# Kernel tuning notes

Measured on AMD Instinct MI355X. Metric: run time of the kernel, lower is better.

Reference implementation:

```python
import jax, jax.numpy as jnp
import numpy as np

NUM_HEADS = 8
NUM_GROUPS = 8
EPS = 1e-5


def group_norm(x, scale, bias):
    # x: [B, C, H, W]; GroupNorm with NUM_GROUPS groups, per-channel affine.
    B, C, H, W = x.shape
    xg = x.reshape(B, NUM_GROUPS, C // NUM_GROUPS, H, W)
    mean = jnp.mean(xg, axis=(2, 3, 4), keepdims=True)
    var = jnp.var(xg, axis=(2, 3, 4), keepdims=True)
    xg = (xg - mean) * jax.lax.rsqrt(var + EPS)
    xn = xg.reshape(B, C, H, W)
    return xn * scale[None, :, None, None] + bias[None, :, None, None]


def setup_inputs() -> dict:
    key = jax.random.key(0)
    ks = jax.random.split(key, 4)
    B, C, H, W = 8, 256, 32, 32
    x = jax.random.normal(ks[0], (B, C, H, W), dtype=jnp.float32)
    gn_scale = jnp.ones((C,), dtype=jnp.float32)
    gn_bias = jnp.zeros((C,), dtype=jnp.float32)
    w_qkv = jax.random.normal(ks[1], (3 * C, C), dtype=jnp.float32) * (1.0 / np.sqrt(C))
    b_qkv = jnp.zeros((3 * C,), dtype=jnp.float32)
    w_out = jax.random.normal(ks[2], (C, C), dtype=jnp.float32) * (1.0 / np.sqrt(C))
    b_out = jnp.zeros((C,), dtype=jnp.float32)
    return {"x": x, "gn_scale": gn_scale, "gn_bias": gn_bias,
            "w_qkv": w_qkv, "b_qkv": b_qkv, "w_out": w_out, "b_out": b_out}


def reference(x, gn_scale, gn_bias, w_qkv, b_qkv, w_out, b_out):
    B, C, H, W = x.shape
    hd = C // NUM_HEADS  # head_dim
    N = H * W

    h = group_norm(x, gn_scale, gn_bias)
    # 1x1 conv == channel matmul: [B, 3C, H, W]
    qkv = jnp.einsum('oc,bchw->bohw', w_qkv, h) + b_qkv[None, :, None, None]
    q, k, v = jnp.split(qkv, 3, axis=1)
    # [B, heads, head_dim, N]
    q = q.reshape(B, NUM_HEADS, hd, N)
    k = k.reshape(B, NUM_HEADS, hd, N)
    v = v.reshape(B, NUM_HEADS, hd, N)

    scale = 1.0 / np.sqrt(hd).astype(np.float32)
    attn = jnp.einsum('bhdn,bhdm->bhnm', q, k) * scale  # [B, h, N, N]
    attn = jax.nn.softmax(attn, axis=-1)
    out = jnp.einsum('bhnm,bhdm->bhdn', attn, v)  # [B, h, hd, N]
    out = out.reshape(B, C, H, W)
    out = jnp.einsum('oc,bchw->bohw', w_out, out) + b_out[None, :, None, None]
    return x + out
```

## Files before the change

kernel.cpp:

```cpp
#include <hip/hip_runtime.h>
#include <hip/hip_bf16.h>
#include <math.h>

#define BB 8
#define CC 256
#define NN 1024
#define HEADS 8
#define HDIM 32
#define NGRP 8

using bf16x8 = __attribute__((ext_vector_type(8))) short;
using f32x4  = __attribute__((ext_vector_type(4))) float;

#if __has_builtin(__builtin_amdgcn_exp2f)
#define EXP2(x) __builtin_amdgcn_exp2f(x)
#else
#define EXP2(x) exp2f(x)
#endif

#define SCL_Q_LOG2E 0.2550348892803828f

static __device__ __forceinline__ ushort f2bf(float x) {
  union { __hip_bfloat16 b; ushort u; } c;
  c.b = __float2bfloat16(x);
  return c.u;
}

__global__ __launch_bounds__(256) void wcast_kernel(
    const float* __restrict__ wqkv, const float* __restrict__ wout,
    ushort* __restrict__ wbf)
{
  const int gid = blockIdx.x * 256 + threadIdx.x;
  const int e8 = gid * 8;
  const float* src = (e8 < 196608) ? (wqkv + e8) : (wout + (e8 - 196608));
  const float4 a = *(const float4*)src;
  const float4 c = *(const float4*)(src + 4);
  union { uint4 v; ushort s[8]; } o;
  o.s[0] = f2bf(a.x); o.s[1] = f2bf(a.y); o.s[2] = f2bf(a.z); o.s[3] = f2bf(a.w);
  o.s[4] = f2bf(c.x); o.s[5] = f2bf(c.y); o.s[6] = f2bf(c.z); o.s[7] = f2bf(c.w);
  *(uint4*)(wbf + e8) = o.v;
}

__global__ __launch_bounds__(256) void gn_stats1(
    const float* __restrict__ x, float2* __restrict__ part)
{
  const int p = blockIdx.x, t = threadIdx.x;
  const float4* src = (const float4*)x + (size_t)p * 512;
  const float4 a = src[t], b = src[t + 256];
  float s  = a.x + a.y + a.z + a.w + b.x + b.y + b.z + b.w;
  float ss = a.x*a.x + a.y*a.y + a.z*a.z + a.w*a.w
           + b.x*b.x + b.y*b.y + b.z*b.z + b.w*b.w;
#pragma unroll
  for (int off = 32; off > 0; off >>= 1) {
    s  += __shfl_down(s, off);
    ss += __shfl_down(ss, off);
  }
  __shared__ float rs[4], rss[4];
  const int wid = t >> 6, lane = t & 63;
  if (lane == 0) { rs[wid] = s; rss[wid] = ss; }
  __syncthreads();
  if (t == 0) {
    float2 o;
    o.x = rs[0] + rs[1] + rs[2] + rs[3];
    o.y = rss[0] + rss[1] + rss[2] + rss[3];
    part[p] = o;
  }
}

__global__ __launch_bounds__(64) void gn_stats2(
    const float2* __restrict__ part, float2* __restrict__ stats)
{
  const int g = blockIdx.x, l = threadIdx.x;
  float s = 0.f, ss = 0.f;
  if (l < 16) { const float2 pp = part[g * 16 + l]; s = pp.x; ss = pp.y; }
#pragma unroll
  for (int off = 8; off > 0; off >>= 1) {
    s  += __shfl_down(s, off);
    ss += __shfl_down(ss, off);
  }
  if (l == 0) {
    const float mean = s * (1.f / 32768.f);
    const float var = ss * (1.f / 32768.f) - mean * mean;
    float2 o; o.x = mean; o.y = rsqrtf(var + 1e-5f);
    stats[g] = o;
  }
}

__global__ __launch_bounds__(256) void gnt_kernel(
    const float* __restrict__ x, const float2* __restrict__ stats,
    const float* __restrict__ gns, const float* __restrict__ gnb,
    ushort* __restrict__ hT)
{
  __shared__ ushort Ls[64 * 68];
  const int t = threadIdx.x;
  const int b = blockIdx.z;
  const int c0 = blockIdx.y << 6, n0 = blockIdx.x << 6;

#pragma unroll
  for (int li = 0; li < 4; ++li) {
    const int id = t + (li << 8);
    const int row = id >> 4, col4 = id & 15;
    const int c = c0 + row;
    const float2 st = stats[b * 8 + (c >> 5)];
    const float sc = gns[c] * st.y;
    const float sh = gnb[c] - st.x * sc;
    const float4 v = *(const float4*)(x + ((size_t)b * CC + c) * NN + n0 + col4 * 4);
    const int nb = col4 * 4;
    Ls[(nb + 0) * 68 + row] = f2bf(v.x * sc + sh);
    Ls[(nb + 1) * 68 + row] = f2bf(v.y * sc + sh);
    Ls[(nb + 2) * 68 + row] = f2bf(v.z * sc + sh);
    Ls[(nb + 3) * 68 + row] = f2bf(v.w * sc + sh);
  }
  __syncthreads();
#pragma unroll
  for (int li = 0; li < 2; ++li) {
    const int id = t + (li << 8);
    const int nR = id >> 3, cP = id & 7;
    union { uint4 v; ushort4 s[2]; } ov;
    ov.s[0] = *(const ushort4*)&Ls[nR * 68 + cP * 8];
    ov.s[1] = *(const ushort4*)&Ls[nR * 68 + cP * 8 + 4];
    *(uint4*)(hT + ((size_t)b * NN + n0 + nR) * CC + c0 + cP * 8) = ov.v;
  }
}

template <int MODE>
__global__ __launch_bounds__(256) void conv_mfma_kernel(
    const ushort* __restrict__ Wbf, const float* __restrict__ bias,
    const ushort* __restrict__ X, const float* __restrict__ xres,
    ushort* __restrict__ qT, ushort* __restrict__ kT, ushort* __restrict__ vN,
    float* __restrict__ out)
{
  const int t = threadIdx.x;
  const int w = t >> 6, l = t & 63;
  const int lg = l >> 4, lr = l & 15;
  const int wr = w >> 1, wc = w & 1;
  const int b = blockIdx.z;
  const int o0 = blockIdx.y << 6, n0 = blockIdx.x << 6;

  __shared__ ushort Ws[64][72];
  __shared__ ushort Xs[64][72];

  union FragU { ushort4 u[2]; bf16x8 f; };
  f32x4 acc[2][2] = {};

  const ushort* Xb = X + (size_t)b * 1024 * 256;

  for (int k0 = 0; k0 < 256; k0 += 64) {
    __syncthreads();
#pragma unroll
    for (int li = 0; li < 2; ++li) {
      const int id = t + (li << 8);
      const int rr = id >> 3, c8 = id & 7;
      const uint4 wv = *(const uint4*)(Wbf + (size_t)(o0 + rr) * 256 + k0 + c8 * 8);
      *(uint4*)&Ws[rr][c8 * 8] = wv;
      const uint4 xv = *(const uint4*)(Xb + (size_t)(n0 + rr) * 256 + k0 + c8 * 8);
      *(uint4*)&Xs[rr][c8 * 8] = xv;
    }
    __syncthreads();

    FragU af[2][2], xf[2][2];
#pragma unroll
    for (int i = 0; i < 2; ++i)
#pragma unroll
      for (int kc = 0; kc < 2; ++kc) {
        const ushort* p = &Ws[wr * 32 + i * 16 + lr][kc * 32 + lg * 4];
        af[i][kc].u[0] = *(const ushort4*)p;
        af[i][kc].u[1] = *(const ushort4*)(p + 16);
        const ushort* q = &Xs[wc * 32 + i * 16 + lr][kc * 32 + lg * 4];
        xf[i][kc].u[0] = *(const ushort4*)q;
        xf[i][kc].u[1] = *(const ushort4*)(q + 16);
      }
#pragma unroll
    for (int ms = 0; ms < 2; ++ms)
#pragma unroll
      for (int ns = 0; ns < 2; ++ns) {
        acc[ms][ns] = __builtin_amdgcn_mfma_f32_16x16x32_bf16(af[ms][0].f, xf[ns][0].f, acc[ms][ns], 0, 0, 0);
        acc[ms][ns] = __builtin_amdgcn_mfma_f32_16x16x32_bf16(af[ms][1].f, xf[ns][1].f, acc[ms][ns], 0, 0, 0);
      }
  }

  if (MODE == 0) {
    const int sec = o0 >> 8;
    const float scl = (sec == 0) ? SCL_Q_LOG2E : 1.0f;
#pragma unroll
    for (int ms = 0; ms < 2; ++ms) {
      const int ob = o0 + wr * 32 + ms * 16 + lg * 4;
      const float4 b4 = *(const float4*)(bias + ob);
      const int oo = ob & 255;
      const int hh = oo >> 5, d0 = oo & 31;
      const int bh = b * 8 + hh;
#pragma unroll
      for (int ns = 0; ns < 2; ++ns) {
        const int n = n0 + wc * 32 + ns * 16 + lr;
        float v0 = (acc[ms][ns][0] + b4.x) * scl;
        float v1 = (acc[ms][ns][1] + b4.y) * scl;
        float v2 = (acc[ms][ns][2] + b4.z) * scl;
        float v3 = (acc[ms][ns][3] + b4.w) * scl;
        if (sec < 2) {
          ushort* dst = (sec == 0) ? qT : kT;
          ushort4 w4 = {f2bf(v0), f2bf(v1), f2bf(v2), f2bf(v3)};
          *(ushort4*)&dst[((size_t)bh * 1024 + n) * 32 + d0] = w4;
        } else {
          vN[((size_t)bh * 32 + d0 + 0) * 1024 + n] = f2bf(v0);
          vN[((size_t)bh * 32 + d0 + 1) * 1024 + n] = f2bf(v1);
          vN[((size_t)bh * 32 + d0 + 2) * 1024 + n] = f2bf(v2);
          vN[((size_t)bh * 32 + d0 + 3) * 1024 + n] = f2bf(v3);
        }
      }
    }
  } else {
#pragma unroll
    for (int ms = 0; ms < 2; ++ms) {
      const int ob = o0 + wr * 32 + ms * 16 + lg * 4;
      const float4 b4 = *(const float4*)(bias + ob);
#pragma unroll
      for (int ns = 0; ns < 2; ++ns) {
        const int n = n0 + wc * 32 + ns * 16 + lr;
        const size_t i0 = ((size_t)b * 256 + ob) * 1024 + n;
        out[i0]          = acc[ms][ns][0] + b4.x + xres[i0];
        out[i0 + 1024]   = acc[ms][ns][1] + b4.y + xres[i0 + 1024];
        out[i0 + 2048]   = acc[ms][ns][2] + b4.z + xres[i0 + 2048];
        out[i0 + 3072]   = acc[ms][ns][3] + b4.w + xres[i0 + 3072];
      }
    }
  }
}

__global__ __launch_bounds__(256) void attn_kernel(
    const ushort* __restrict__ qT, const ushort* __restrict__ kT,
    const ushort* __restrict__ vN, ushort* __restrict__ aoT)
{
  const int t = threadIdx.x;
  const int w = t >> 6, l = t & 63;
  const int lg = l >> 4, lr = l & 15;
  const int bh = blockIdx.y;
  const int b = bh >> 3, hh = bh & 7;
  const int qbase = blockIdx.x << 6;

  __shared__ ushort Ks[128][40];
  __shared__ ushort Vs[32][136];

  union FragU { ushort4 u[2]; bf16x8 f; };

  FragU qf;
  {
    const ushort* Qp = qT + (((size_t)bh * 1024 + qbase + w * 16 + lr) * 32) + lg * 4;
    qf.u[0] = *(const ushort4*)Qp;
    qf.u[1] = *(const ushort4*)(Qp + 16);
  }

  f32x4 accO[2] = {};
  float m_st = -1e30f, l_st = 0.f;

  const ushort* Kbh = kT + (size_t)bh * 1024 * 32;
  const ushort* Vbh = vN + (size_t)bh * 32 * 1024;
  const uint4* Kt = (const uint4*)Kbh;
  const int vd = t >> 4, vm8 = (t & 15) * 8;

  uint4 kr0, kr1, vr0, vr1;
  {
    kr0 = Kt[t];
    kr1 = Kt[t + 256];
    vr0 = *(const uint4*)(Vbh + (size_t)vd * 1024 + vm8);
    vr1 = *(const uint4*)(Vbh + (size_t)(vd + 16) * 1024 + vm8);
  }

  for (int m0 = 0; m0 < NN; m0 += 128) {
    __syncthreads();
    *(uint4*)&Ks[t >> 2][(t & 3) * 8] = kr0;
    *(uint4*)&Ks[64 + (t >> 2)][(t & 3) * 8] = kr1;
    *(uint4*)&Vs[vd][vm8] = vr0;
    *(uint4*)&Vs[vd + 16][vm8] = vr1;
    __syncthreads();

    if (m0 + 128 < NN) {
      const int mn = m0 + 128;
      kr0 = Kt[mn * 4 + t];
      kr1 = Kt[mn * 4 + t + 256];
      vr0 = *(const uint4*)(Vbh + (size_t)vd * 1024 + mn + vm8);
      vr1 = *(const uint4*)(Vbh + (size_t)(vd + 16) * 1024 + mn + vm8);
    }

    f32x4 s[8];
#pragma unroll
    for (int ms = 0; ms < 8; ++ms) {
      FragU kf;
      const ushort* kp = &Ks[ms * 16 + lr][lg * 4];
      kf.u[0] = *(const ushort4*)kp;
      kf.u[1] = *(const ushort4*)(kp + 16);
      f32x4 z = {0.f, 0.f, 0.f, 0.f};
      s[ms] = __builtin_amdgcn_mfma_f32_16x16x32_bf16(kf.f, qf.f, z, 0, 0, 0);
    }

    float mx = s[0][0];
#pragma unroll
    for (int ms = 0; ms < 8; ++ms)
#pragma unroll
      for (int r = 0; r < 4; ++r) mx = fmaxf(mx, s[ms][r]);
    mx = fmaxf(mx, __shfl_xor(mx, 16));
    mx = fmaxf(mx, __shfl_xor(mx, 32));
    const float mnew = fmaxf(m_st, mx);
    const float c = EXP2(m_st - mnew);
    m_st = mnew;
    float ls = 0.f;
#pragma unroll
    for (int ms = 0; ms < 8; ++ms)
#pragma unroll
      for (int r = 0; r < 4; ++r) {
        const float p = EXP2(s[ms][r] - mnew);
        s[ms][r] = p;
        ls += p;
      }
    ls += __shfl_xor(ls, 16);
    ls += __shfl_xor(ls, 32);
    l_st = l_st * c + ls;
#pragma unroll
    for (int dt = 0; dt < 2; ++dt)
#pragma unroll
      for (int r = 0; r < 4; ++r) accO[dt][r] *= c;

    bf16x8 pb[4];
#pragma unroll
    for (int mc = 0; mc < 4; ++mc) {
      bf16x8 f;
#pragma unroll
      for (int r = 0; r < 4; ++r) {
        f[r]     = (short)f2bf(s[2 * mc][r]);
        f[r + 4] = (short)f2bf(s[2 * mc + 1][r]);
      }
      pb[mc] = f;
    }

#pragma unroll
    for (int dt = 0; dt < 2; ++dt) {
#pragma unroll
      for (int mc = 0; mc < 4; ++mc) {
        FragU vf;
        const ushort* vp = &Vs[dt * 16 + lr][mc * 32 + lg * 4];
        vf.u[0] = *(const ushort4*)vp;
        vf.u[1] = *(const ushort4*)(vp + 16);
        accO[dt] = __builtin_amdgcn_mfma_f32_16x16x32_bf16(vf.f, pb[mc], accO[dt], 0, 0, 0);
      }
    }
  }

  const float inv = 1.f / l_st;
  const int n = qbase + w * 16 + lr;
  ushort* ap = aoT + ((size_t)b * 1024 + n) * 256 + hh * 32 + lg * 4;
#pragma unroll
  for (int dt = 0; dt < 2; ++dt) {
    ushort4 w4;
    w4.x = f2bf(accO[dt][0] * inv);
    w4.y = f2bf(accO[dt][1] * inv);
    w4.z = f2bf(accO[dt][2] * inv);
    w4.w = f2bf(accO[dt][3] * inv);
    *(ushort4*)(ap + dt * 16) = w4;
  }
}

extern "C" void kernel_launch(void* const* d_in, const int* in_sizes, int n_in,
                              void* d_out, int out_size, void* d_ws, size_t ws_size,
                              hipStream_t stream)
{
  const float* x    = (const float*)d_in[0];
  const float* gns  = (const float*)d_in[1];
  const float* gnb  = (const float*)d_in[2];
  const float* wqkv = (const float*)d_in[3];
  const float* bqkv = (const float*)d_in[4];
  const float* wout = (const float*)d_in[5];
  const float* bout = (const float*)d_in[6];
  float* out = (float*)d_out;

  char* ws = (char*)d_ws;
  ushort* hT    = (ushort*)(ws);
  ushort* qT    = (ushort*)(ws + (4u << 20));
  ushort* kT    = (ushort*)(ws + (8u << 20));
  ushort* vN    = (ushort*)(ws + (12u << 20));
  ushort* aoT   = (ushort*)(ws + (16u << 20));
  ushort* wbf   = (ushort*)(ws + (20u << 20));
  float2* part  = (float2*)(ws + (21u << 20));
  float2* stats = (float2*)(ws + (21u << 20) + 8192);

  wcast_kernel<<<dim3(128), dim3(256), 0, stream>>>(wqkv, wout, wbf);
  gn_stats1<<<dim3(1024), dim3(256), 0, stream>>>(x, part);
  gn_stats2<<<dim3(64), dim3(64), 0, stream>>>(part, stats);
  gnt_kernel<<<dim3(16, 4, 8), dim3(256), 0, stream>>>(x, stats, gns, gnb, hT);
  conv_mfma_kernel<0><<<dim3(16, 12, 8), dim3(256), 0, stream>>>(
      wbf, bqkv, hT, nullptr, qT, kT, vN, nullptr);
  attn_kernel<<<dim3(16, 64), dim3(256), 0, stream>>>(qT, kT, vN, aoT);
  conv_mfma_kernel<1><<<dim3(16, 4, 8), dim3(256), 0, stream>>>(
      wbf + 768 * 256, bout, aoT, x, nullptr, nullptr, nullptr, out);
}
```

Measured before the change: 128.1 us.

## Fuse weight cast and GN stats into consumers, stage stores through LDS

Removes the separate weight-cast and group-norm finalize kernels. The bf16 weight conversion moves into the conv tile loader, and the stats reduction moves into gnt_kernel, cutting two launches. The QKV conv epilogue now goes through shared memory so q/k/v writes are wide and coalesced, with q/k stored in a split half-head layout the attention kernel reads directly. The attention output is also staged through LDS for 16-byte stores, and the softmax max/sum reductions are split into independent chains for more ILP. The cost is that each conv block redoes the fp32-to-bf16 weight conversion and reads fp32 weights, which doubles weight traffic.

```diff
diff --git a/kernel.cpp b/kernel.cpp
--- a/kernel.cpp
+++ b/kernel.cpp
@@ -24,21 +24,6 @@
   union { __hip_bfloat16 b; ushort u; } c;
   c.b = __float2bfloat16(x);
   return c.u;
-}
-
-__global__ __launch_bounds__(256) void wcast_kernel(
-    const float* __restrict__ wqkv, const float* __restrict__ wout,
-    ushort* __restrict__ wbf)
-{
-  const int gid = blockIdx.x * 256 + threadIdx.x;
-  const int e8 = gid * 8;
-  const float* src = (e8 < 196608) ? (wqkv + e8) : (wout + (e8 - 196608));
-  const float4 a = *(const float4*)src;
-  const float4 c = *(const float4*)(src + 4);
-  union { uint4 v; ushort s[8]; } o;
-  o.s[0] = f2bf(a.x); o.s[1] = f2bf(a.y); o.s[2] = f2bf(a.z); o.s[3] = f2bf(a.w);
-  o.s[4] = f2bf(c.x); o.s[5] = f2bf(c.y); o.s[6] = f2bf(c.z); o.s[7] = f2bf(c.w);
-  *(uint4*)(wbf + e8) = o.v;
 }
 
 __global__ __launch_bounds__(256) void gn_stats1(
@@ -67,41 +52,41 @@
   }
 }
 
-__global__ __launch_bounds__(64) void gn_stats2(
-    const float2* __restrict__ part, float2* __restrict__ stats)
-{
-  const int g = blockIdx.x, l = threadIdx.x;
-  float s = 0.f, ss = 0.f;
-  if (l < 16) { const float2 pp = part[g * 16 + l]; s = pp.x; ss = pp.y; }
-#pragma unroll
-  for (int off = 8; off > 0; off >>= 1) {
-    s  += __shfl_down(s, off);
-    ss += __shfl_down(ss, off);
-  }
-  if (l == 0) {
-    const float mean = s * (1.f / 32768.f);
-    const float var = ss * (1.f / 32768.f) - mean * mean;
-    float2 o; o.x = mean; o.y = rsqrtf(var + 1e-5f);
-    stats[g] = o;
-  }
-}
-
 __global__ __launch_bounds__(256) void gnt_kernel(
-    const float* __restrict__ x, const float2* __restrict__ stats,
+    const float* __restrict__ x, const float2* __restrict__ part,
     const float* __restrict__ gns, const float* __restrict__ gnb,
     ushort* __restrict__ hT)
 {
   __shared__ ushort Ls[64 * 68];
+  __shared__ float2 gstat[2];
   const int t = threadIdx.x;
   const int b = blockIdx.z;
   const int c0 = blockIdx.y << 6, n0 = blockIdx.x << 6;
+
+  if (t < 32) {
+    const int gsel = t >> 4, ci = t & 15;
+    const float2 pp = part[((b * 8) + (blockIdx.y << 1) + gsel) * 16 + ci];
+    float s = pp.x, ss = pp.y;
+#pragma unroll
+    for (int off = 8; off > 0; off >>= 1) {
+      s  += __shfl_down(s, off, 16);
+      ss += __shfl_down(ss, off, 16);
+    }
+    if (ci == 0) {
+      const float mean = s * (1.f / 32768.f);
+      const float var = ss * (1.f / 32768.f) - mean * mean;
+      float2 o; o.x = mean; o.y = rsqrtf(var + 1e-5f);
+      gstat[gsel] = o;
+    }
+  }
+  __syncthreads();
 
 #pragma unroll
   for (int li = 0; li < 4; ++li) {
     const int id = t + (li << 8);
     const int row = id >> 4, col4 = id & 15;
     const int c = c0 + row;
-    const float2 st = stats[b * 8 + (c >> 5)];
+    const float2 st = gstat[row >> 5];
     const float sc = gns[c] * st.y;
     const float sh = gnb[c] - st.x * sc;
     const float4 v = *(const float4*)(x + ((size_t)b * CC + c) * NN + n0 + col4 * 4);
@@ -125,9 +110,9 @@
 
 template <int MODE>
 __global__ __launch_bounds__(256) void conv_mfma_kernel(
-    const ushort* __restrict__ Wbf, const float* __restrict__ bias,
+    const float* __restrict__ W32, const float* __restrict__ bias,
     const ushort* __restrict__ X, const float* __restrict__ xres,
-    ushort* __restrict__ qT, ushort* __restrict__ kT, ushort* __restrict__ vN,
+    ushort* __restrict__ qT2, ushort* __restrict__ kT2, ushort* __restrict__ vN,
     float* __restrict__ out)
 {
   const int t = threadIdx.x;
@@ -151,8 +136,13 @@
     for (int li = 0; li < 2; ++li) {
       const int id = t + (li << 8);
       const int rr = id >> 3, c8 = id & 7;
-      const uint4 wv = *(const uint4*)(Wbf + (size_t)(o0 + rr) * 256 + k0 + c8 * 8);
-      *(uint4*)&Ws[rr][c8 * 8] = wv;
+      const float* wsrc = W32 + (size_t)(o0 + rr) * 256 + k0 + c8 * 8;
+      const float4 wa = *(const float4*)wsrc;
+      const float4 wb = *(const float4*)(wsrc + 4);
+      union { uint4 v; ushort s[8]; } wv;
+      wv.s[0] = f2bf(wa.x); wv.s[1] = f2bf(wa.y); wv.s[2] = f2bf(wa.z); wv.s[3] = f2bf(wa.w);
+      wv.s[4] = f2bf(wb.x); wv.s[5] = f2bf(wb.y); wv.s[6] = f2bf(wb.z); wv.s[7] = f2bf(wb.w);
+      *(uint4*)&Ws[rr][c8 * 8] = wv.v;
       const uint4 xv = *(const uint4*)(Xb + (size_t)(n0 + rr) * 256 + k0 + c8 * 8);
       *(uint4*)&Xs[rr][c8 * 8] = xv;
     }
@@ -181,32 +171,47 @@
 
   if (MODE == 0) {
     const int sec = o0 >> 8;
+    const int oin = o0 & 255;
     const float scl = (sec == 0) ? SCL_Q_LOG2E : 1.0f;
+    ushort* Lp = &Xs[0][0];
+    __syncthreads();
 #pragma unroll
     for (int ms = 0; ms < 2; ++ms) {
       const int ob = o0 + wr * 32 + ms * 16 + lg * 4;
       const float4 b4 = *(const float4*)(bias + ob);
-      const int oo = ob & 255;
-      const int hh = oo >> 5, d0 = oo & 31;
-      const int bh = b * 8 + hh;
+      const int ol = wr * 32 + ms * 16 + lg * 4;
 #pragma unroll
       for (int ns = 0; ns < 2; ++ns) {
-        const int n = n0 + wc * 32 + ns * 16 + lr;
-        float v0 = (acc[ms][ns][0] + b4.x) * scl;
-        float v1 = (acc[ms][ns][1] + b4.y) * scl;
-        float v2 = (acc[ms][ns][2] + b4.z) * scl;
-        float v3 = (acc[ms][ns][3] + b4.w) * scl;
-        if (sec < 2) {
-          ushort* dst = (sec == 0) ? qT : kT;
-          ushort4 w4 = {f2bf(v0), f2bf(v1), f2bf(v2), f2bf(v3)};
-          *(ushort4*)&dst[((size_t)bh * 1024 + n) * 32 + d0] = w4;
-        } else {
-          vN[((size_t)bh * 32 + d0 + 0) * 1024 + n] = f2bf(v0);
-          vN[((size_t)bh * 32 + d0 + 1) * 1024 + n] = f2bf(v1);
-          vN[((size_t)bh * 32 + d0 + 2) * 1024 + n] = f2bf(v2);
-          vN[((size_t)bh * 32 + d0 + 3) * 1024 + n] = f2bf(v3);
-        }
-      }
+        const int nl = wc * 32 + ns * 16 + lr;
+        Lp[(ol + 0) * 68 + nl] = f2bf((acc[ms][ns][0] + b4.x) * scl);
+        Lp[(ol + 1) * 68 + nl] = f2bf((acc[ms][ns][1] + b4.y) * scl);
+        Lp[(ol + 2) * 68 + nl] = f2bf((acc[ms][ns][2] + b4.z) * scl);
+        Lp[(ol + 3) * 68 + nl] = f2bf((acc[ms][ns][3] + b4.w) * scl);
+      }
+    }
+    __syncthreads();
+    if (sec < 2) {
+      ushort* dst = (sec == 0) ? qT2 : kT2;
+      const int nl = t & 63, hd = t >> 6;
+      const int hl = hd >> 1, dh = hd & 1;
+      const int bh = b * 8 + (oin >> 5) + hl;
+      union { uint4 v[2]; ushort s[16]; } o;
+#pragma unroll
+      for (int j = 0; j < 16; ++j)
+        o.s[j] = Lp[(hl * 32 + dh * 16 + j) * 68 + nl];
+      uint4* dp = (uint4*)(dst + (((size_t)bh * 2 + dh) * 1024 + n0 + nl) * 16);
+      dp[0] = o.v[0];
+      dp[1] = o.v[1];
+    } else {
+      const int r = t >> 2, p = t & 3;
+      const int oo = oin + r, hh = oo >> 5, d0 = oo & 31;
+      union { uint4 v[2]; ushort4 s[4]; } o;
+#pragma unroll
+      for (int j = 0; j < 4; ++j)
+        o.s[j] = *(const ushort4*)&Lp[r * 68 + p * 16 + j * 4];
+      uint4* dp = (uint4*)(vN + (((size_t)b * 8 + hh) * 32 + d0) * 1024 + n0 + p * 16);
+      dp[0] = o.v[0];
+      dp[1] = o.v[1];
     }
   } else {
 #pragma unroll
@@ -227,7 +232,7 @@
 }
 
 __global__ __launch_bounds__(256) void attn_kernel(
-    const ushort* __restrict__ qT, const ushort* __restrict__ kT,
+    const ushort* __restrict__ qT2, const ushort* __restrict__ kT2,
     const ushort* __restrict__ vN, ushort* __restrict__ aoT)
 {
   const int t = threadIdx.x;
@@ -242,41 +247,42 @@
 
   union FragU { ushort4 u[2]; bf16x8 f; };
 
+  const ushort* Qb2 = qT2 + (size_t)bh * 2 * 1024 * 16;
+  const ushort* Kb2 = kT2 + (size_t)bh * 2 * 1024 * 16;
+  const ushort* Vbh = vN + (size_t)bh * 32 * 1024;
+
   FragU qf;
   {
-    const ushort* Qp = qT + (((size_t)bh * 1024 + qbase + w * 16 + lr) * 32) + lg * 4;
-    qf.u[0] = *(const ushort4*)Qp;
-    qf.u[1] = *(const ushort4*)(Qp + 16);
+    const int qn = qbase + w * 16 + lr;
+    qf.u[0] = *(const ushort4*)(Qb2 + (size_t)qn * 16 + lg * 4);
+    qf.u[1] = *(const ushort4*)(Qb2 + (size_t)(1024 + qn) * 16 + lg * 4);
   }
 
   f32x4 accO[2] = {};
   float m_st = -1e30f, l_st = 0.f;
 
-  const ushort* Kbh = kT + (size_t)bh * 1024 * 32;
-  const ushort* Vbh = vN + (size_t)bh * 32 * 1024;
-  const uint4* Kt = (const uint4*)Kbh;
+  const int km = t >> 2, kq = t & 3;
+  const size_t koff0 = ((size_t)(kq >> 1) * 1024 + km) * 16 + (kq & 1) * 8;
   const int vd = t >> 4, vm8 = (t & 15) * 8;
 
   uint4 kr0, kr1, vr0, vr1;
-  {
-    kr0 = Kt[t];
-    kr1 = Kt[t + 256];
-    vr0 = *(const uint4*)(Vbh + (size_t)vd * 1024 + vm8);
-    vr1 = *(const uint4*)(Vbh + (size_t)(vd + 16) * 1024 + vm8);
-  }
+  kr0 = *(const uint4*)(Kb2 + koff0);
+  kr1 = *(const uint4*)(Kb2 + koff0 + 64 * 16);
+  vr0 = *(const uint4*)(Vbh + (size_t)vd * 1024 + vm8);
+  vr1 = *(const uint4*)(Vbh + (size_t)(vd + 16) * 1024 + vm8);
 
   for (int m0 = 0; m0 < NN; m0 += 128) {
     __syncthreads();
-    *(uint4*)&Ks[t >> 2][(t & 3) * 8] = kr0;
-    *(uint4*)&Ks[64 + (t >> 2)][(t & 3) * 8] = kr1;
+    *(uint4*)&Ks[km][kq * 8] = kr0;
+    *(uint4*)&Ks[64 + km][kq * 8] = kr1;
     *(uint4*)&Vs[vd][vm8] = vr0;
     *(uint4*)&Vs[vd + 16][vm8] = vr1;
     __syncthreads();
 
     if (m0 + 128 < NN) {
       const int mn = m0 + 128;
-      kr0 = Kt[mn * 4 + t];
-      kr1 = Kt[mn * 4 + t + 256];
+      kr0 = *(const uint4*)(Kb2 + koff0 + (size_t)mn * 16);
+      kr1 = *(const uint4*)(Kb2 + koff0 + (size_t)(mn + 64) * 16);
       vr0 = *(const uint4*)(Vbh + (size_t)vd * 1024 + mn + vm8);
       vr1 = *(const uint4*)(Vbh + (size_t)(vd + 16) * 1024 + mn + vm8);
     }
@@ -292,25 +298,32 @@
       s[ms] = __builtin_amdgcn_mfma_f32_16x16x32_bf16(kf.f, qf.f, z, 0, 0, 0);
     }
 
-    float mx = s[0][0];
-#pragma unroll
-    for (int ms = 0; ms < 8; ++ms)
-#pragma unroll
-      for (int r = 0; r < 4; ++r) mx = fmaxf(mx, s[ms][r]);
+    float pm0 = s[0][0], pm1 = s[0][1], pm2 = s[0][2], pm3 = s[0][3];
+#pragma unroll
+    for (int ms = 1; ms < 8; ++ms) {
+      pm0 = fmaxf(pm0, s[ms][0]);
+      pm1 = fmaxf(pm1, s[ms][1]);
+      pm2 = fmaxf(pm2, s[ms][2]);
+      pm3 = fmaxf(pm3, s[ms][3]);
+    }
+    float mx = fmaxf(fmaxf(pm0, pm1), fmaxf(pm2, pm3));
     mx = fmaxf(mx, __shfl_xor(mx, 16));
     mx = fmaxf(mx, __shfl_xor(mx, 32));
     const float mnew = fmaxf(m_st, mx);
     const float c = EXP2(m_st - mnew);
     m_st = mnew;
-    float ls = 0.f;
-#pragma unroll
-    for (int ms = 0; ms < 8; ++ms)
-#pragma unroll
-      for (int r = 0; r < 4; ++r) {
-        const float p = EXP2(s[ms][r] - mnew);
-        s[ms][r] = p;
-        ls += p;
-      }
+
+    float ls0 = 0.f, ls1 = 0.f, ls2 = 0.f, ls3 = 0.f;
+#pragma unroll
+    for (int ms = 0; ms < 8; ++ms) {
+      const float p0 = EXP2(s[ms][0] - mnew);
+      const float p1 = EXP2(s[ms][1] - mnew);
+      const float p2 = EXP2(s[ms][2] - mnew);
+      const float p3 = EXP2(s[ms][3] - mnew);
+      s[ms][0] = p0; s[ms][1] = p1; s[ms][2] = p2; s[ms][3] = p3;
+      ls0 += p0; ls1 += p1; ls2 += p2; ls3 += p3;
+    }
+    float ls = (ls0 + ls1) + (ls2 + ls3);
     ls += __shfl_xor(ls, 16);
     ls += __shfl_xor(ls, 32);
     l_st = l_st * c + ls;
@@ -345,16 +358,20 @@
   }
 
   const float inv = 1.f / l_st;
-  const int n = qbase + w * 16 + lr;
-  ushort* ap = aoT + ((size_t)b * 1024 + n) * 256 + hh * 32 + lg * 4;
-#pragma unroll
-  for (int dt = 0; dt < 2; ++dt) {
-    ushort4 w4;
-    w4.x = f2bf(accO[dt][0] * inv);
-    w4.y = f2bf(accO[dt][1] * inv);
-    w4.z = f2bf(accO[dt][2] * inv);
-    w4.w = f2bf(accO[dt][3] * inv);
-    *(ushort4*)(ap + dt * 16) = w4;
+  ushort* Lb = &Ks[0][0];
+  __syncthreads();
+#pragma unroll
+  for (int dt = 0; dt < 2; ++dt)
+#pragma unroll
+    for (int r = 0; r < 4; ++r)
+      Lb[(w * 16 + lr) * 36 + dt * 16 + lg * 4 + r] = f2bf(accO[dt][r] * inv);
+  __syncthreads();
+  {
+    const int nl = t >> 2, p = t & 3;
+    union { uint4 v; ushort4 s[2]; } o;
+    o.s[0] = *(const ushort4*)&Lb[nl * 36 + p * 8];
+    o.s[1] = *(const ushort4*)&Lb[nl * 36 + p * 8 + 4];
+    *(uint4*)(aoT + ((size_t)b * 1024 + qbase + nl) * 256 + hh * 32 + p * 8) = o.v;
   }
 }
 
@@ -372,22 +389,18 @@
   float* out = (float*)d_out;
 
   char* ws = (char*)d_ws;
-  ushort* hT    = (ushort*)(ws);
-  ushort* qT    = (ushort*)(ws + (4u << 20));
-  ushort* kT    = (ushort*)(ws + (8u << 20));
-  ushort* vN    = (ushort*)(ws + (12u << 20));
-  ushort* aoT   = (ushort*)(ws + (16u << 20));
-  ushort* wbf   = (ushort*)(ws + (20u << 20));
-  float2* part  = (float2*)(ws + (21u << 20));
-  float2* stats = (float2*)(ws + (21u << 20) + 8192);
-
-  wcast_kernel<<<dim3(128), dim3(256), 0, stream>>>(wqkv, wout, wbf);
+  ushort* hT   = (ushort*)(ws);
+  ushort* qT2  = (ushort*)(ws + (4u << 20));
+  ushort* kT2  = (ushort*)(ws + (8u << 20));
+  ushort* vN   = (ushort*)(ws + (12u << 20));
+  ushort* aoT  = (ushort*)(ws + (16u << 20));
+  float2* part = (float2*)(ws + (20u << 20));
+
   gn_stats1<<<dim3(1024), dim3(256), 0, stream>>>(x, part);
-  gn_stats2<<<dim3(64), dim3(64), 0, stream>>>(part, stats);
-  gnt_kernel<<<dim3(16, 4, 8), dim3(256), 0, stream>>>(x, stats, gns, gnb, hT);
+  gnt_kernel<<<dim3(16, 4, 8), dim3(256), 0, stream>>>(x, part, gns, gnb, hT);
   conv_mfma_kernel<0><<<dim3(16, 12, 8), dim3(256), 0, stream>>>(
-      wbf, bqkv, hT, nullptr, qT, kT, vN, nullptr);
-  attn_kernel<<<dim3(16, 64), dim3(256), 0, stream>>>(qT, kT, vN, aoT);
+      wqkv, bqkv, hT, nullptr, qT2, kT2, vN, nullptr);
+  attn_kernel<<<dim3(16, 64), dim3(256), 0, stream>>>(qT2, kT2, vN, aoT);
   conv_mfma_kernel<1><<<dim3(16, 4, 8), dim3(256), 0, stream>>>(
-      wbf + 768 * 256, bout, aoT, x, nullptr, nullptr, nullptr, out);
-}
+      wout, bout, aoT, x, nullptr, nullptr, nullptr, out);
+}
```

After: 125.8 us. Within noise of the previous version (-1.8%).
